# Performance work log

Hardware: AMD Instinct MI355X
Metric: run time of the kernel (lower is better)

## Reference

```python
import jax, jax.numpy as jnp
import numpy as np

N_NODES = 50000
N_EDGES = 800000
IN_C = 128
HID = 128
OUT_C = 64
N_GRAPHS = 256


def setup_inputs() -> dict:
    key = jax.random.key(0)
    ks = jax.random.split(key, 12)
    x = jax.random.normal(ks[0], (N_NODES, IN_C), dtype=jnp.float32)
    edge_index = jax.random.randint(ks[1], (2, N_EDGES), 0, N_NODES, dtype=jnp.int32)
    batch = jnp.sort(jax.random.randint(ks[2], (N_NODES,), 0, N_GRAPHS, dtype=jnp.int32))
    def lin(k, fan_in, fan_out):
        bound = 1.0 / np.sqrt(fan_in)
        kw, kb = jax.random.split(k)
        W = jax.random.uniform(kw, (fan_in, fan_out), minval=-bound, maxval=bound, dtype=jnp.float32)
        b = jax.random.uniform(kb, (fan_out,), minval=-bound, maxval=bound, dtype=jnp.float32)
        return W, b
    W1a, b1a = lin(ks[3], IN_C, HID)
    W1b, b1b = lin(ks[4], HID, HID)
    W2a, b2a = lin(ks[5], HID, HID)
    W2b, b2b = lin(ks[6], HID, HID)
    Wl, bl = lin(ks[7], HID, OUT_C)
    return {"x": x, "edge_index": edge_index, "batch": batch,
            "W1a": W1a, "b1a": b1a, "W1b": W1b, "b1b": b1b,
            "W2a": W2a, "b2a": b2a, "W2b": W2b, "b2b": b2b,
            "Wl": Wl, "bl": bl}


def gin_conv(x, edge_index, Wa, ba, Wb, bb):
    # GINConv with eps=0: h_i = MLP(x_i + sum_{j->i} x_j)
    src, dst = edge_index[0], edge_index[1]
    agg = jax.ops.segment_sum(x[src], dst, num_segments=x.shape[0])  # [N, d]
    h = x + agg
    h = jax.nn.relu(h @ Wa + ba) @ Wb + bb
    return h


def reference(x, edge_index, batch, W1a, b1a, W1b, b1b, W2a, b2a, W2b, b2b, Wl, bl):
    h = gin_conv(x, edge_index, W1a, b1a, W1b, b1b)
    h = gin_conv(h, edge_index, W2a, b2a, W2b, b2b)
    # global mean pool over graphs in the batch
    sums = jax.ops.segment_sum(h, batch, num_segments=N_GRAPHS)          # [G, HID]
    cnts = jax.ops.segment_sum(jnp.ones((h.shape[0],), h.dtype), batch, num_segments=N_GRAPHS)
    pooled = sums / jnp.maximum(cnts, 1.0)[:, None]
    return pooled @ Wl + bl  # [G, OUT_C]
```

## Files before the change

kernel.cpp:

```cpp
#include <hip/hip_runtime.h>

constexpr int N  = 50000;
constexpr int E  = 800000;
constexpr int C  = 128;
constexpr int G  = 256;
constexpr int OC = 64;
constexpr int D  = 64;

constexpr int NBUCK = 196;
constexpr int BCAP  = 5120;
constexpr int EPB = 2048;
constexpr int EB  = (E + EPB - 1) / EPB;
constexpr int WB1 = 64;
constexpr int WXB = 64;
constexpr int WHB = 32;
constexpr int GB  = (N + 255) / 256;

typedef __attribute__((ext_vector_type(8))) short short8;
typedef __attribute__((ext_vector_type(4))) float f32x4;
typedef __attribute__((ext_vector_type(2))) float f32x2;

__device__ __forceinline__ unsigned int au(float f) { return __float_as_uint(f); }

__device__ __forceinline__ unsigned short f2bf(float f) {
    unsigned int u = au(f);
    u += 0x7fffu + ((u >> 16) & 1u);
    return (unsigned short)(u >> 16);
}
__device__ __forceinline__ unsigned int pack_bf16(float lo, float hi) {
    return ((au(hi) + 0x8000u) & 0xFFFF0000u) | ((au(lo) + 0x8000u) >> 16);
}

__device__ __forceinline__ void acc16(f32x2* a, uint4 v) {
    a[0] += __builtin_amdgcn_cvt_pk_f32_fp8((int)v.x, false);
    a[1] += __builtin_amdgcn_cvt_pk_f32_fp8((int)v.x, true);
    a[2] += __builtin_amdgcn_cvt_pk_f32_fp8((int)v.y, false);
    a[3] += __builtin_amdgcn_cvt_pk_f32_fp8((int)v.y, true);
    a[4] += __builtin_amdgcn_cvt_pk_f32_fp8((int)v.z, false);
    a[5] += __builtin_amdgcn_cvt_pk_f32_fp8((int)v.z, true);
    a[6] += __builtin_amdgcn_cvt_pk_f32_fp8((int)v.w, false);
    a[7] += __builtin_amdgcn_cvt_pk_f32_fp8((int)v.w, true);
}
__device__ __forceinline__ void set16(f32x2* a, uint4 v) {
    a[0] = __builtin_amdgcn_cvt_pk_f32_fp8((int)v.x, false);
    a[1] = __builtin_amdgcn_cvt_pk_f32_fp8((int)v.x, true);
    a[2] = __builtin_amdgcn_cvt_pk_f32_fp8((int)v.y, false);
    a[3] = __builtin_amdgcn_cvt_pk_f32_fp8((int)v.y, true);
    a[4] = __builtin_amdgcn_cvt_pk_f32_fp8((int)v.z, false);
    a[5] = __builtin_amdgcn_cvt_pk_f32_fp8((int)v.z, true);
    a[6] = __builtin_amdgcn_cvt_pk_f32_fp8((int)v.w, false);
    a[7] = __builtin_amdgcn_cvt_pk_f32_fp8((int)v.w, true);
}

__device__ __forceinline__ void gather_rows(f32x2* a, const uint4* F16,
                                            const unsigned short* irow, int dg, int l) {
    const uint2* i2 = (const uint2*)irow;
    int nb  = dg >> 2;
    int rem = dg & 3;
    if (nb > 0) {
        uint2 iu = i2[0];
        int t0 = (int)(iu.x & 0xffffu), t1 = (int)(iu.x >> 16);
        int t2 = (int)(iu.y & 0xffffu), t3 = (int)(iu.y >> 16);
        uint4 v0 = F16[(size_t)t0 * 8 + l];
        uint4 v1 = F16[(size_t)t1 * 8 + l];
        uint4 v2 = F16[(size_t)t2 * 8 + l];
        uint4 v3 = F16[(size_t)t3 * 8 + l];
        for (int b = 1; b < nb; ++b) {
            uint2 ju = i2[b];
            int u0 = (int)(ju.x & 0xffffu), u1 = (int)(ju.x >> 16);
            int u2 = (int)(ju.y & 0xffffu), u3 = (int)(ju.y >> 16);
            uint4 w0 = F16[(size_t)u0 * 8 + l];
            uint4 w1 = F16[(size_t)u1 * 8 + l];
            uint4 w2 = F16[(size_t)u2 * 8 + l];
            uint4 w3 = F16[(size_t)u3 * 8 + l];
            acc16(a, v0); acc16(a, v1); acc16(a, v2); acc16(a, v3);
            v0 = w0; v1 = w1; v2 = w2; v3 = w3;
        }
        acc16(a, v0); acc16(a, v1); acc16(a, v2); acc16(a, v3);
    }
    if (rem) {
        const unsigned short* ir = irow + nb * 4;
#pragma unroll
        for (int m = 0; m < 3; ++m) {
            if (m < rem) {
                uint4 v = F16[(size_t)ir[m] * 8 + l];
                acc16(a, v);
            }
        }
    }
}


__global__ __launch_bounds__(256) void build_prep_kernel(const int* __restrict__ src,
                                                         const int* __restrict__ dst,
                                                         int* __restrict__ bcount,
                                                         unsigned int* __restrict__ bucketbuf,
                                                         const float* __restrict__ W1a,
                                                         const float* __restrict__ W1b,
                                                         const float* __restrict__ W2a,
                                                         const float* __restrict__ W2b,
                                                         const float* __restrict__ Wl,
                                                         const float* __restrict__ bl,
                                                         const float* __restrict__ b1b,
                                                         const float* __restrict__ b2b,
                                                         unsigned short* __restrict__ wt1a,
                                                         unsigned short* __restrict__ wtx,
                                                         float* __restrict__ Whead,
                                                         float* __restrict__ c1,
                                                         float* __restrict__ bhead,
                                                         const int* __restrict__ batch,
                                                         int* __restrict__ gcnt) {
    int b = blockIdx.x;
    int tid = threadIdx.x;
    if (b < EB) {
        __shared__ int lcount[NBUCK];
        __shared__ int lbase[NBUCK];
        __shared__ int lcur[NBUCK];
        for (int i = tid; i < NBUCK; i += 256) { lcount[i] = 0; lcur[i] = 0; }
        __syncthreads();
        int e0 = b * EPB;
        int sv[8], dv[8];
#pragma unroll
        for (int i = 0; i < 8; ++i) {
            int e = e0 + i * 256 + tid;
            if (e < E) {
                sv[i] = src[e];
                dv[i] = dst[e];
                atomicAdd(&lcount[dv[i] >> 8], 1);
            } else {
                dv[i] = -1;
            }
        }
        __syncthreads();
        if (tid < NBUCK) {
            int c = lcount[tid];
            lbase[tid] = (c > 0) ? atomicAdd(&bcount[tid], c) : 0;
        }
        __syncthreads();
#pragma unroll
        for (int i = 0; i < 8; ++i) {
            if (dv[i] >= 0) {
                int bk = dv[i] >> 8;
                int pos = lbase[bk] + atomicAdd(&lcur[bk], 1);
                if (pos < BCAP)
                    bucketbuf[(size_t)bk * BCAP + pos] =
                        ((unsigned int)sv[i] << 16) | (unsigned int)(dv[i] & 255);
            }
        }
    } else if (b < EB + WB1) {
        int idx = (b - EB) * 256 + tid;
        int n = idx >> 7, k = idx & 127;
        wt1a[idx] = f2bf(W1a[k * 128 + n]);
    } else if (b < EB + WB1 + WXB) {
        int idx = (b - EB - WB1) * 256 + tid;
        int i = idx >> 7, j = idx & 127;
        float acc = 0.f;
        for (int k = 0; k < 128; ++k) acc += W1b[i * 128 + k] * W2a[k * 128 + j];
        wtx[j * 128 + i] = f2bf(acc);
    } else if (b < EB + WB1 + WXB + WHB) {
        int idx = (b - EB - WB1 - WXB) * 256 + tid;
        int i = idx >> 6, j = idx & 63;
        float acc = 0.f;
        for (int k = 0; k < 128; ++k) acc += W2b[i * 128 + k] * Wl[k * OC + j];
        Whead[i * OC + j] = acc;
    } else if (b == EB + WB1 + WXB + WHB) {
        if (tid < 128) {
            float acc = 0.f;
            for (int k = 0; k < 128; ++k) acc += b1b[k] * W2a[k * 128 + tid];
            c1[tid] = acc;
        } else if (tid < 192) {
            int j = tid - 128;
            float acc = bl[j];
            for (int k = 0; k < 128; ++k) acc += b2b[k] * Wl[k * OC + j];
            bhead[j] = acc;
        }
    } else {
        __shared__ int h[G];
        h[tid] = 0;
        __syncthreads();
        int i = (b - (EB + WB1 + WXB + WHB + 1)) * 256 + tid;
        if (i < N) atomicAdd(&h[batch[i]], 1);
        __syncthreads();
        int c = h[tid];
        if (c > 0) atomicAdd(&gcnt[tid], c);
    }
}


__global__ __launch_bounds__(256) void bucket_fill_kernel(const int* __restrict__ bcount,
                                                          const unsigned int* __restrict__ bucketbuf,
                                                          unsigned short* __restrict__ ell,
                                                          int* __restrict__ deg) {
    __shared__ int lcur[256];
    int b = blockIdx.x;
    int tid = threadIdx.x;
    lcur[tid] = 0;
    __syncthreads();
    int cnt = min(bcount[b], BCAP);
    const unsigned int* buf = bucketbuf + (size_t)b * BCAP;
    int nbase = b << 8;
    for (int i = tid; i < cnt; i += 256) {
        unsigned int e = buf[i];
        int dlow = (int)(e & 255u);
        int p = atomicAdd(&lcur[dlow], 1);
        if (p < D) ell[(size_t)(nbase + dlow) * D + p] = (unsigned short)(e >> 16);
    }
    __syncthreads();
    int node = nbase + tid;
    if (node < N) deg[node] = lcur[tid];
}


__global__ __launch_bounds__(256, 4) void gemma_kernel(const float* __restrict__ x,
                                                       const unsigned short* __restrict__ wt1a,
                                                       unsigned char* __restrict__ z1) {
    constexpr int LD = 136;
    __shared__ short Xl[64 * LD];
    __shared__ short Wl[128 * LD];
    int tid = threadIdx.x;
    int lane = tid & 63, wave = tid >> 6;
    int row0 = blockIdx.x * 64;

    const short8* Wg = (const short8*)wt1a;
#pragma unroll
    for (int i = tid; i < 2048; i += 256) {
        int r = i >> 4, c = i & 15;
        *((short8*)(Wl + r * LD) + c) = Wg[i];
    }
    const float4* x4 = (const float4*)(x + (size_t)row0 * C);
#pragma unroll
    for (int i = tid; i < 2048; i += 256) {
        int r = i >> 5, c4 = i & 31;
        float4 v = (row0 + r < N) ? x4[i] : make_float4(0.f, 0.f, 0.f, 0.f);
        uint2 u;
        u.x = pack_bf16(v.x, v.y);
        u.y = pack_bf16(v.z, v.w);
        *(uint2*)(Xl + r * LD + c4 * 4) = u;
    }

    int mw = wave >> 1, nw = wave & 1;
    int lid = lane & 15, quad = lane >> 4;
    f32x4 acc[2][4];
#pragma unroll
    for (int nt = 0; nt < 4; ++nt) {
        acc[0][nt] = (f32x4){0.f, 0.f, 0.f, 0.f};
        acc[1][nt] = (f32x4){0.f, 0.f, 0.f, 0.f};
    }
    __syncthreads();

#pragma unroll
    for (int ks = 0; ks < 4; ++ks) {
        short8 a0 = *(const short8*)(Xl + (mw * 32 + lid) * LD + ks * 32 + quad * 8);
        short8 a1 = *(const short8*)(Xl + (mw * 32 + 16 + lid) * LD + ks * 32 + quad * 8);
#pragma unroll
        for (int nt = 0; nt < 4; ++nt) {
            short8 bf = *(const short8*)(Wl + (nw * 64 + nt * 16 + lid) * LD + ks * 32 + quad * 8);
            acc[0][nt] = __builtin_amdgcn_mfma_f32_16x16x32_bf16(a0, bf, acc[0][nt], 0, 0, 0);
            acc[1][nt] = __builtin_amdgcn_mfma_f32_16x16x32_bf16(a1, bf, acc[1][nt], 0, 0, 0);
        }
    }

#pragma unroll
    for (int mt = 0; mt < 2; ++mt) {
#pragma unroll
        for (int nt = 0; nt < 4; ++nt) {
            int mbase = row0 + mw * 32 + mt * 16 + quad * 4;
            int n = nw * 64 + nt * 16 + lid;
            f32x4 v = acc[mt][nt];
#pragma unroll
            for (int r = 0; r < 4; ++r) {
                int row = mbase + r;
                if (row < N) {
                    unsigned int p = (unsigned int)__builtin_amdgcn_cvt_pk_fp8_f32(v[r], 0.f, 0, false);
                    z1[(size_t)row * 128 + n] = (unsigned char)(p & 0xFF);
                }
            }
        }
    }
}


__global__ __launch_bounds__(512, 6) void k2_kernel(const unsigned char* __restrict__ z1,
                                                    const int* __restrict__ deg,
                                                    const unsigned short* __restrict__ ell,
                                                    const unsigned short* __restrict__ wtx,
                                                    const float* __restrict__ b1a,
                                                    unsigned char* __restrict__ z2) {
    constexpr int LD = 136;
    __shared__ short Xl[64 * LD];
    __shared__ short Wl[128 * LD];
    int tid = threadIdx.x;
    int lane = tid & 63, wave = tid >> 6;
    int row0 = blockIdx.x * 64;

    const short8* Wg = (const short8*)wtx;
#pragma unroll
    for (int i = tid; i < 2048; i += 512) {
        int r = i >> 4, c = i & 15;
        *((short8*)(Wl + r * LD) + c) = Wg[i];
    }

    {
        int grp = tid >> 3;
        int l   = tid & 7;
        const uint4* F16 = (const uint4*)z1;
        int n = row0 + grp;
        f32x2 a[8];
        if (n < N) {
            int dgc = min(deg[n], D);
            set16(a, F16[(size_t)n * 8 + l]);
            gather_rows(a, F16, ell + (size_t)n * D, dgc, l);
            const f32x2* bp = (const f32x2*)(b1a + l * 16);
#pragma unroll
            for (int q = 0; q < 8; ++q) {
                a[q] += bp[q];
                a[q].x = fmaxf(a[q].x, 0.f);
                a[q].y = fmaxf(a[q].y, 0.f);
            }
        } else {
#pragma unroll
            for (int q = 0; q < 8; ++q) a[q] = (f32x2){0.f, 0.f};
        }
        uint4 o0, o1;
        o0.x = pack_bf16(a[0].x, a[0].y); o0.y = pack_bf16(a[1].x, a[1].y);
        o0.z = pack_bf16(a[2].x, a[2].y); o0.w = pack_bf16(a[3].x, a[3].y);
        o1.x = pack_bf16(a[4].x, a[4].y); o1.y = pack_bf16(a[5].x, a[5].y);
        o1.z = pack_bf16(a[6].x, a[6].y); o1.w = pack_bf16(a[7].x, a[7].y);
        uint4* xp = (uint4*)(Xl + grp * LD + l * 16);
        xp[0] = o0;
        xp[1] = o1;
    }

    int mw = wave >> 2, nw = wave & 3;
    int lid = lane & 15, quad = lane >> 4;
    f32x4 acc[2][2];
#pragma unroll
    for (int nt = 0; nt < 2; ++nt) {
        acc[0][nt] = (f32x4){0.f, 0.f, 0.f, 0.f};
        acc[1][nt] = (f32x4){0.f, 0.f, 0.f, 0.f};
    }
    __syncthreads();

#pragma unroll
    for (int ks = 0; ks < 4; ++ks) {
        short8 a0 = *(const short8*)(Xl + (mw * 32 + lid) * LD + ks * 32 + quad * 8);
        short8 a1 = *(const short8*)(Xl + (mw * 32 + 16 + lid) * LD + ks * 32 + quad * 8);
#pragma unroll
        for (int nt = 0; nt < 2; ++nt) {
            short8 bf = *(const short8*)(Wl + (nw * 32 + nt * 16 + lid) * LD + ks * 32 + quad * 8);
            acc[0][nt] = __builtin_amdgcn_mfma_f32_16x16x32_bf16(a0, bf, acc[0][nt], 0, 0, 0);
            acc[1][nt] = __builtin_amdgcn_mfma_f32_16x16x32_bf16(a1, bf, acc[1][nt], 0, 0, 0);
        }
    }

#pragma unroll
    for (int mt = 0; mt < 2; ++mt) {
#pragma unroll
        for (int nt = 0; nt < 2; ++nt) {
            int mbase = row0 + mw * 32 + mt * 16 + quad * 4;
            int n = nw * 32 + nt * 16 + lid;
            f32x4 v = acc[mt][nt];
#pragma unroll
            for (int r = 0; r < 4; ++r) {
                int row = mbase + r;
                if (row < N) {
                    unsigned int p = (unsigned int)__builtin_amdgcn_cvt_pk_fp8_f32(v[r], 0.f, 0, false);
                    z2[(size_t)row * 128 + n] = (unsigned char)(p & 0xFF);
                }
            }
        }
    }
}


__global__ __launch_bounds__(512, 6) void k3_kernel(const unsigned char* __restrict__ z2,
                                                    const int* __restrict__ deg,
                                                    const unsigned short* __restrict__ ell,
                                                    const float* __restrict__ c1,
                                                    const float* __restrict__ b2a,
                                                    const int* __restrict__ batch,
                                                    float* __restrict__ gsum) {
    constexpr int LD = 136;
    __shared__ short Xl[64 * LD];
    int tid = threadIdx.x;
    int lane = tid & 63, wave = tid >> 6;
    int row0 = blockIdx.x * 64;

    {
        int grp = tid >> 3;
        int l   = tid & 7;
        const uint4* F16 = (const uint4*)z2;
        int n = row0 + grp;
        f32x2 a[8];
        if (n < N) {
            int dfull = deg[n];
            int dgc = min(dfull, D);
            set16(a, F16[(size_t)n * 8 + l]);
            gather_rows(a, F16, ell + (size_t)n * D, dgc, l);
            float degf = (float)(1 + dfull);
            const f32x2* c1p = (const f32x2*)(c1 + l * 16);
            const f32x2* b2p = (const f32x2*)(b2a + l * 16);
#pragma unroll
            for (int q = 0; q < 8; ++q) {
                a[q] += degf * c1p[q] + b2p[q];
                a[q].x = fmaxf(a[q].x, 0.f);
                a[q].y = fmaxf(a[q].y, 0.f);
            }
        } else {
#pragma unroll
            for (int q = 0; q < 8; ++q) a[q] = (f32x2){0.f, 0.f};
        }
        uint4 o0, o1;
        o0.x = pack_bf16(a[0].x, a[0].y); o0.y = pack_bf16(a[1].x, a[1].y);
        o0.z = pack_bf16(a[2].x, a[2].y); o0.w = pack_bf16(a[3].x, a[3].y);
        o1.x = pack_bf16(a[4].x, a[4].y); o1.y = pack_bf16(a[5].x, a[5].y);
        o1.z = pack_bf16(a[6].x, a[6].y); o1.w = pack_bf16(a[7].x, a[7].y);
        uint4* xp = (uint4*)(Xl + grp * LD + l * 16);
        xp[0] = o0;
        xp[1] = o1;
    }
    __syncthreads();

    int r0 = wave * 8;
    int gprev = -1;
    float a0 = 0.f, a1 = 0.f;
    for (int rr = 0; rr < 8; ++rr) {
        int row = row0 + r0 + rr;
        if (row >= N) break;
        int g = batch[row];
        if (g != gprev) {
            if (gprev >= 0) {
                atomicAdd(&gsum[gprev * C + 2 * lane], a0);
                atomicAdd(&gsum[gprev * C + 2 * lane + 1], a1);
            }
            gprev = g; a0 = 0.f; a1 = 0.f;
        }
        unsigned int pv = *(const unsigned int*)(Xl + (r0 + rr) * LD + 2 * lane);
        a0 += __uint_as_float((pv & 0xffffu) << 16);
        a1 += __uint_as_float(pv & 0xffff0000u);
    }
    if (gprev >= 0) {
        atomicAdd(&gsum[gprev * C + 2 * lane], a0);
        atomicAdd(&gsum[gprev * C + 2 * lane + 1], a1);
    }
}


__global__ __launch_bounds__(64) void head_kernel(const float* __restrict__ gsum,
                                                  const int* __restrict__ gcnt,
                                                  const float* __restrict__ Whead,
                                                  const float* __restrict__ bhead,
                                                  float* __restrict__ out) {
    int g = blockIdx.x;
    int t = threadIdx.x;
    __shared__ float pooled[C];
    float inv = 1.0f / (float)max(gcnt[g], 1);
    pooled[t]      = gsum[g * C + t] * inv;
    pooled[t + 64] = gsum[g * C + 64 + t] * inv;
    __syncthreads();
    float o = bhead[t];
#pragma unroll 4
    for (int k = 0; k < C; ++k) o += pooled[k] * Whead[k * OC + t];
    out[g * OC + t] = o;
}


extern "C" void kernel_launch(void* const* d_in, const int* in_sizes, int n_in,
                              void* d_out, int out_size, void* d_ws, size_t ws_size,
                              hipStream_t stream) {
    const float* x    = (const float*)d_in[0];
    const int*   ei   = (const int*)d_in[1];
    const int*   bat  = (const int*)d_in[2];
    const float* W1a  = (const float*)d_in[3];
    const float* b1a  = (const float*)d_in[4];
    const float* W1b  = (const float*)d_in[5];
    const float* b1b  = (const float*)d_in[6];
    const float* W2a  = (const float*)d_in[7];
    const float* b2a  = (const float*)d_in[8];
    const float* W2b  = (const float*)d_in[9];
    const float* b2b  = (const float*)d_in[10];
    const float* Wl   = (const float*)d_in[11];
    const float* bl   = (const float*)d_in[12];
    float*       out  = (float*)d_out;

    float* gsum    = (float*)d_ws;
    int*   gcnt    = (int*)(gsum + G * C);
    int*   bcount  = gcnt + G;
    int*   deg     = bcount + NBUCK;
    unsigned int*   bucketbuf = (unsigned int*)(deg + N);
    unsigned short* ell  = (unsigned short*)(bucketbuf + (size_t)NBUCK * BCAP);
    unsigned short* wt1a = ell + (size_t)N * D;
    unsigned short* wtx  = wt1a + 16384;
    float* Whead = (float*)(wtx + 16384);
    float* c1    = Whead + 128 * OC;
    float* bhead = c1 + 128;
    unsigned char* z1 = (unsigned char*)(bhead + OC);
    unsigned char* z2 = z1 + (size_t)N * 128;

    const int* src = ei;
    const int* dst = ei + E;

    hipMemsetAsync(gsum, 0, (size_t)(G * C + G + NBUCK) * sizeof(int), stream);

    build_prep_kernel<<<EB + WB1 + WXB + WHB + 1 + GB, 256, 0, stream>>>(
        src, dst, bcount, bucketbuf, W1a, W1b, W2a, W2b, Wl, bl, b1b, b2b,
        wt1a, wtx, Whead, c1, bhead, bat, gcnt);

    bucket_fill_kernel<<<NBUCK, 256, 0, stream>>>(bcount, bucketbuf, ell, deg);

    int mb = (N + 63) / 64;

    gemma_kernel<<<mb, 256, 0, stream>>>(x, wt1a, z1);
    k2_kernel<<<mb, 512, 0, stream>>>(z1, deg, ell, wtx, b1a, z2);
    k3_kernel<<<mb, 512, 0, stream>>>(z2, deg, ell, c1, b2a, bat, gsum);
    head_kernel<<<G, 64, 0, stream>>>(gsum, gcnt, Whead, bhead, out);
}
```

Before: 197.1 us.

## Merge bucket fill with first GEMM and degree-sort gather rows per tile

Combines the bucket-fill and first-layer GEMM kernels into one launch, selecting the role by block index so the two independent stages run together and one launch is saved. The GEMM half moves to 512 threads with 8 waves, each covering 32 columns. In k2 and k3, each 64-row tile now sorts its rows by degree with a wave-level rank computation, so the 8-lane groups inside a wave gather rows of similar length, which reduces divergence in the neighbor loop. The sort adds a sync and some shuffle work to every block.

```diff
diff --git a/kernel.cpp b/kernel.cpp
--- a/kernel.cpp
+++ b/kernel.cpp
@@ -15,6 +15,8 @@
 constexpr int WXB = 64;
 constexpr int WHB = 32;
 constexpr int GB  = (N + 255) / 256;
+constexpr int FB  = NBUCK;
+constexpr int MB  = (N + 63) / 64;
 
 typedef __attribute__((ext_vector_type(8))) short short8;
 typedef __attribute__((ext_vector_type(4))) float f32x4;
@@ -87,6 +89,20 @@
                 acc16(a, v);
             }
         }
+    }
+}
+
+__device__ __forceinline__ void tile_sort(short* sorted, const int* deg, int row0,
+                                          int lane, int wave) {
+    if (wave == 0) {
+        int n0 = row0 + lane;
+        int key = (n0 < N) ? min(deg[n0], D) : -1;
+        int rank = 0;
+        for (int j = 0; j < 64; ++j) {
+            int kj = __shfl(key, j);
+            rank += (kj < key) || (kj == key && j < lane);
+        }
+        sorted[rank] = (short)lane;
     }
 }
 
@@ -187,49 +203,50 @@
 }
 
 
-__global__ __launch_bounds__(256) void bucket_fill_kernel(const int* __restrict__ bcount,
-                                                          const unsigned int* __restrict__ bucketbuf,
-                                                          unsigned short* __restrict__ ell,
-                                                          int* __restrict__ deg) {
-    __shared__ int lcur[256];
-    int b = blockIdx.x;
+__global__ __launch_bounds__(512, 6) void mid_kernel(const int* __restrict__ bcount,
+                                                     const unsigned int* __restrict__ bucketbuf,
+                                                     unsigned short* __restrict__ ell,
+                                                     int* __restrict__ deg,
+                                                     const float* __restrict__ x,
+                                                     const unsigned short* __restrict__ wt1a,
+                                                     unsigned char* __restrict__ z1) {
     int tid = threadIdx.x;
-    lcur[tid] = 0;
-    __syncthreads();
-    int cnt = min(bcount[b], BCAP);
-    const unsigned int* buf = bucketbuf + (size_t)b * BCAP;
-    int nbase = b << 8;
-    for (int i = tid; i < cnt; i += 256) {
-        unsigned int e = buf[i];
-        int dlow = (int)(e & 255u);
-        int p = atomicAdd(&lcur[dlow], 1);
-        if (p < D) ell[(size_t)(nbase + dlow) * D + p] = (unsigned short)(e >> 16);
-    }
-    __syncthreads();
-    int node = nbase + tid;
-    if (node < N) deg[node] = lcur[tid];
-}
-
-
-__global__ __launch_bounds__(256, 4) void gemma_kernel(const float* __restrict__ x,
-                                                       const unsigned short* __restrict__ wt1a,
-                                                       unsigned char* __restrict__ z1) {
+    if (blockIdx.x < FB) {
+        __shared__ int lcur[256];
+        int b = blockIdx.x;
+        if (tid < 256) lcur[tid] = 0;
+        __syncthreads();
+        int cnt = min(bcount[b], BCAP);
+        const unsigned int* buf = bucketbuf + (size_t)b * BCAP;
+        int nbase = b << 8;
+        for (int i = tid; i < cnt; i += 512) {
+            unsigned int e = buf[i];
+            int dlow = (int)(e & 255u);
+            int p = atomicAdd(&lcur[dlow], 1);
+            if (p < D) ell[(size_t)(nbase + dlow) * D + p] = (unsigned short)(e >> 16);
+        }
+        __syncthreads();
+        if (tid < 256) {
+            int node = nbase + tid;
+            if (node < N) deg[node] = lcur[tid];
+        }
+        return;
+    }
     constexpr int LD = 136;
     __shared__ short Xl[64 * LD];
     __shared__ short Wl[128 * LD];
-    int tid = threadIdx.x;
     int lane = tid & 63, wave = tid >> 6;
-    int row0 = blockIdx.x * 64;
+    int row0 = (blockIdx.x - FB) * 64;
 
     const short8* Wg = (const short8*)wt1a;
 #pragma unroll
-    for (int i = tid; i < 2048; i += 256) {
+    for (int i = tid; i < 2048; i += 512) {
         int r = i >> 4, c = i & 15;
         *((short8*)(Wl + r * LD) + c) = Wg[i];
     }
     const float4* x4 = (const float4*)(x + (size_t)row0 * C);
 #pragma unroll
-    for (int i = tid; i < 2048; i += 256) {
+    for (int i = tid; i < 2048; i += 512) {
         int r = i >> 5, c4 = i & 31;
         float4 v = (row0 + r < N) ? x4[i] : make_float4(0.f, 0.f, 0.f, 0.f);
         uint2 u;
@@ -238,11 +255,11 @@
         *(uint2*)(Xl + r * LD + c4 * 4) = u;
     }
 
-    int mw = wave >> 1, nw = wave & 1;
+    int mw = wave >> 2, nw = wave & 3;
     int lid = lane & 15, quad = lane >> 4;
-    f32x4 acc[2][4];
-#pragma unroll
-    for (int nt = 0; nt < 4; ++nt) {
+    f32x4 acc[2][2];
+#pragma unroll
+    for (int nt = 0; nt < 2; ++nt) {
         acc[0][nt] = (f32x4){0.f, 0.f, 0.f, 0.f};
         acc[1][nt] = (f32x4){0.f, 0.f, 0.f, 0.f};
     }
@@ -253,8 +270,8 @@
         short8 a0 = *(const short8*)(Xl + (mw * 32 + lid) * LD + ks * 32 + quad * 8);
         short8 a1 = *(const short8*)(Xl + (mw * 32 + 16 + lid) * LD + ks * 32 + quad * 8);
 #pragma unroll
-        for (int nt = 0; nt < 4; ++nt) {
-            short8 bf = *(const short8*)(Wl + (nw * 64 + nt * 16 + lid) * LD + ks * 32 + quad * 8);
+        for (int nt = 0; nt < 2; ++nt) {
+            short8 bf = *(const short8*)(Wl + (nw * 32 + nt * 16 + lid) * LD + ks * 32 + quad * 8);
             acc[0][nt] = __builtin_amdgcn_mfma_f32_16x16x32_bf16(a0, bf, acc[0][nt], 0, 0, 0);
             acc[1][nt] = __builtin_amdgcn_mfma_f32_16x16x32_bf16(a1, bf, acc[1][nt], 0, 0, 0);
         }
@@ -263,9 +280,9 @@
 #pragma unroll
     for (int mt = 0; mt < 2; ++mt) {
 #pragma unroll
-        for (int nt = 0; nt < 4; ++nt) {
+        for (int nt = 0; nt < 2; ++nt) {
             int mbase = row0 + mw * 32 + mt * 16 + quad * 4;
-            int n = nw * 64 + nt * 16 + lid;
+            int n = nw * 32 + nt * 16 + lid;
             f32x4 v = acc[mt][nt];
 #pragma unroll
             for (int r = 0; r < 4; ++r) {
@@ -289,6 +306,7 @@
     constexpr int LD = 136;
     __shared__ short Xl[64 * LD];
     __shared__ short Wl[128 * LD];
+    __shared__ short sorted[64];
     int tid = threadIdx.x;
     int lane = tid & 63, wave = tid >> 6;
     int row0 = blockIdx.x * 64;
@@ -299,12 +317,15 @@
         int r = i >> 4, c = i & 15;
         *((short8*)(Wl + r * LD) + c) = Wg[i];
     }
+    tile_sort(sorted, deg, row0, lane, wave);
+    __syncthreads();
 
     {
         int grp = tid >> 3;
         int l   = tid & 7;
+        int lr  = sorted[grp];
         const uint4* F16 = (const uint4*)z1;
-        int n = row0 + grp;
+        int n = row0 + lr;
         f32x2 a[8];
         if (n < N) {
             int dgc = min(deg[n], D);
@@ -326,7 +347,7 @@
         o0.z = pack_bf16(a[2].x, a[2].y); o0.w = pack_bf16(a[3].x, a[3].y);
         o1.x = pack_bf16(a[4].x, a[4].y); o1.y = pack_bf16(a[5].x, a[5].y);
         o1.z = pack_bf16(a[6].x, a[6].y); o1.w = pack_bf16(a[7].x, a[7].y);
-        uint4* xp = (uint4*)(Xl + grp * LD + l * 16);
+        uint4* xp = (uint4*)(Xl + lr * LD + l * 16);
         xp[0] = o0;
         xp[1] = o1;
     }
@@ -382,15 +403,20 @@
                                                     float* __restrict__ gsum) {
     constexpr int LD = 136;
     __shared__ short Xl[64 * LD];
+    __shared__ short sorted[64];
     int tid = threadIdx.x;
     int lane = tid & 63, wave = tid >> 6;
     int row0 = blockIdx.x * 64;
 
+    tile_sort(sorted, deg, row0, lane, wave);
+    __syncthreads();
+
     {
         int grp = tid >> 3;
         int l   = tid & 7;
+        int lr  = sorted[grp];
         const uint4* F16 = (const uint4*)z2;
-        int n = row0 + grp;
+        int n = row0 + lr;
         f32x2 a[8];
         if (n < N) {
             int dfull = deg[n];
@@ -415,7 +441,7 @@
         o0.z = pack_bf16(a[2].x, a[2].y); o0.w = pack_bf16(a[3].x, a[3].y);
         o1.x = pack_bf16(a[4].x, a[4].y); o1.y = pack_bf16(a[5].x, a[5].y);
         o1.z = pack_bf16(a[6].x, a[6].y); o1.w = pack_bf16(a[7].x, a[7].y);
-        uint4* xp = (uint4*)(Xl + grp * LD + l * 16);
+        uint4* xp = (uint4*)(Xl + lr * LD + l * 16);
         xp[0] = o0;
         xp[1] = o1;
     }
@@ -506,12 +532,10 @@
         src, dst, bcount, bucketbuf, W1a, W1b, W2a, W2b, Wl, bl, b1b, b2b,
         wt1a, wtx, Whead, c1, bhead, bat, gcnt);
 
-    bucket_fill_kernel<<<NBUCK, 256, 0, stream>>>(bcount, bucketbuf, ell, deg);
-
-    int mb = (N + 63) / 64;
-
-    gemma_kernel<<<mb, 256, 0, stream>>>(x, wt1a, z1);
-    k2_kernel<<<mb, 512, 0, stream>>>(z1, deg, ell, wtx, b1a, z2);
-    k3_kernel<<<mb, 512, 0, stream>>>(z2, deg, ell, c1, b2a, bat, gsum);
+    mid_kernel<<<FB + MB, 512, 0, stream>>>(bcount, bucketbuf, ell, deg,
+                                            x, wt1a, z1);
+
+    k2_kernel<<<MB, 512, 0, stream>>>(z1, deg, ell, wtx, b1a, z2);
+    k3_kernel<<<MB, 512, 0, stream>>>(z2, deg, ell, c1, b2a, bat, gsum);
     head_kernel<<<G, 64, 0, stream>>>(gsum, gcnt, Whead, bhead, out);
 }
```

After: 191.1 us. -3.0%, faster.
